# Optimization experiments

Hardware: AMD Instinct MI355X
Metric: run time of the kernel (lower is better)

The kernel has to match this reference:

```python
import jax, jax.numpy as jnp
import numpy as np

B, N, D = 8, 2048, 512

def setup_inputs() -> dict:
    key = jax.random.key(0)
    k1, k2, k3, k4, k5 = jax.random.split(key, 5)
    s = 1.0 / np.sqrt(D)
    return {
        "x": jax.random.normal(k1, (B, N, D), dtype=jnp.float32),
        "w_qkv": jax.random.normal(k2, (D, 3 * D), dtype=jnp.float32) * s,
        "b_qkv": jax.random.normal(k3, (3 * D,), dtype=jnp.float32) * 0.01,
        "w_fc": jax.random.normal(k4, (D, D), dtype=jnp.float32) * s,
        "b_fc": jax.random.normal(k5, (D,), dtype=jnp.float32) * 0.01,
    }

def reference(x, w_qkv, b_qkv, w_fc, b_fc):
    scale = 1.0 / (x.shape[-1] ** 0.5)
    qkv = x @ w_qkv + b_qkv                      # [B, N, 3D]
    q, k, v = jnp.split(qkv, 3, axis=-1)         # each [B, N, D]
    attn = jnp.einsum("bnd,bmd->bnm", q, k) * scale
    attn = jax.nn.softmax(attn, axis=-1)
    out = jnp.einsum("bnm,bmd->bnd", attn, v)
    return out @ w_fc + b_fc + x
```

## Files before the change

### kernel.cpp

```cpp
#include <hip/hip_runtime.h>
#include <stdint.h>

typedef unsigned short u16;
typedef unsigned int u32;
typedef __attribute__((ext_vector_type(8))) short short8;
typedef __attribute__((ext_vector_type(4))) float f32x4;
typedef __attribute__((ext_vector_type(8))) unsigned short u16x8;
typedef __attribute__((ext_vector_type(4))) float float4_t;

__device__ __forceinline__ float b2f(u16 u) { return __uint_as_float(((u32)u) << 16); }
__device__ __forceinline__ u16 f2b(float f) {
  u32 u = __float_as_uint(f);
  u += 0x7fffu + ((u >> 16) & 1u);
  return (u16)(u >> 16);
}

typedef const __attribute__((address_space(1))) void* gas_t;
typedef __attribute__((address_space(3))) void* las_t;
__device__ __forceinline__ void gl_lds16(const void* g, void* l) {
  __builtin_amdgcn_global_load_lds((gas_t)(uintptr_t)g, (las_t)(u32)(uintptr_t)l, 16, 0, 0);
}
__device__ __forceinline__ void barrier_pin() {
  __builtin_amdgcn_sched_barrier(0);
  __builtin_amdgcn_s_barrier();
  __builtin_amdgcn_sched_barrier(0);
}

__global__ __launch_bounds__(256) void cvt_f2b_kernel(const float* __restrict__ src,
                                                      u16* __restrict__ dst, long n) {
  long i = ((long)blockIdx.x * 256 + threadIdx.x) * 8;
  if (i >= n) return;
  float4_t v0 = *(const float4_t*)(src + i);
  float4_t v1 = *(const float4_t*)(src + i + 4);
  u16x8 o;
#pragma unroll
  for (int j = 0; j < 4; ++j) { o[j] = f2b(v0[j]); o[4 + j] = f2b(v1[j]); }
  *(u16x8*)(dst + i) = o;
}

__global__ __launch_bounds__(256) void tr_cvt(const float* __restrict__ src,
                                              u16* __restrict__ dst, int R, int C) {
  __shared__ float t[32][33];
  const int bx = blockIdx.x * 32;
  const int by = blockIdx.y * 32;
  const int tx = threadIdx.x & 31, ty = threadIdx.x >> 5;
#pragma unroll
  for (int i = 0; i < 32; i += 8)
    t[ty + i][tx] = src[(long)(by + ty + i) * C + bx + tx];
  __syncthreads();
#pragma unroll
  for (int i = 0; i < 32; i += 8)
    dst[(long)(bx + ty + i) * R + by + tx] = f2b(t[tx][ty + i]);
}

__global__ __launch_bounds__(256) void tr_v(const u16* __restrict__ qkv, u16* __restrict__ vt) {
  __shared__ u16 t[32][33];
  const int b = blockIdx.z;
  const int r0 = blockIdx.x * 32;
  const int d0 = blockIdx.y * 32;
  const int tx = threadIdx.x & 31, ty = threadIdx.x >> 5;
#pragma unroll
  for (int i = 0; i < 32; i += 8)
    t[ty + i][tx] = qkv[((long)b * 2048 + r0 + ty + i) * 1536 + 1024 + d0 + tx];
  __syncthreads();
#pragma unroll
  for (int i = 0; i < 32; i += 8)
    vt[((long)b * 512 + d0 + ty + i) * 2048 + r0 + tx] = t[tx][ty + i];
}

template <int NREP, bool OUT_F32, bool BIAS, bool RES>
__global__ __launch_bounds__(512, 1)
void gemm256(const u16* __restrict__ A, const u16* __restrict__ Bt, void* __restrict__ Cv,
             const float* __restrict__ bias, const float* __restrict__ res,
             int K, int lda, int ldb, int ldc,
             long aStride, long bStride, long cStride, float alpha) {
  __shared__ u16 As[2][256 * 64];
  __shared__ u16 Bs[2][NREP * 64 * 64];
  const int tid = threadIdx.x;
  const int wid = tid >> 6, lane = tid & 63;
  const int wr = wid >> 2, wc = wid & 3;
  const int lr = lane & 15, lg = lane >> 4;

  const int gx = gridDim.x, gy = gridDim.y;
  int id = (blockIdx.z * gy + blockIdx.y) * gx + blockIdx.x;
  const int nwg = gx * gy * gridDim.z;
  id = (id & 7) * (nwg >> 3) + (id >> 3);
  const int bxi = id % gx;
  const int t2 = id / gx;
  const int byi = t2 % gy;
  const long z = t2 / gy;

  A += z * aStride;
  Bt += z * bStride;
  const int by = byi * 256;
  const int bx = bxi * (NREP * 64);

  f32x4 acc[8][NREP] = {};
  short8 bh[NREP][2];

  const int w8l = wid * 8 + (lane >> 3);
  const int scol_src = ((lane & 7) ^ (lane >> 3)) * 8;
  const int scol_lin = (lane & 7) * 8;
  const int nT = K >> 6;
  const int sx = lane & 7;

  auto stage_A = [&](int h, int kt) {
    const int bb = kt & 1;
    const long kc = (long)kt * 64 + scol_src;
#pragma unroll
    for (int r = 0; r < 2; ++r) {
      const int row = h * 128 + r * 64 + w8l;
      gl_lds16(A + (long)(by + row) * lda + kc, &As[bb][row * 64 + scol_lin]);
    }
  };
  auto stage_Bf = [&](int kt) {
    const int bb = kt & 1;
    const long kc = (long)kt * 64 + scol_src;
#pragma unroll
    for (int r = 0; r < NREP; ++r) {
      const int row = r * 64 + w8l;
      gl_lds16(Bt + (long)(bx + row) * ldb + kc, &Bs[bb][row * 64 + scol_lin]);
    }
  };

  auto read_B = [&](int bb) {
#pragma unroll
    for (int n = 0; n < NREP; ++n) {
      const int brow = (NREP == 4) ? ((n >> 1) * 128 + wc * 32 + (n & 1) * 16 + lr)
                                   : (wc * 32 + n * 16 + lr);
#pragma unroll
      for (int ks = 0; ks < 2; ++ks)
        bh[n][ks] = *(const short8*)&Bs[bb][brow * 64 + (((ks * 4 + lg) ^ sx) * 8)];
    }
  };
  auto half_mfma = [&](int bb, int mh) {
    short8 a[4][2];
#pragma unroll
    for (int mi = 0; mi < 4; ++mi)
#pragma unroll
      for (int ks = 0; ks < 2; ++ks)
        a[mi][ks] = *(const short8*)&As[bb][(mh * 128 + wr * 64 + mi * 16 + lr) * 64 +
                                            (((ks * 4 + lg) ^ sx) * 8)];
    __builtin_amdgcn_s_setprio(1);
#pragma unroll
    for (int mi = 0; mi < 4; ++mi)
#pragma unroll
      for (int n = 0; n < NREP; ++n)
#pragma unroll
        for (int ks = 0; ks < 2; ++ks)
          acc[mh * 4 + mi][n] = __builtin_amdgcn_mfma_f32_16x16x32_bf16(
              a[mi][ks], bh[n][ks], acc[mh * 4 + mi][n], 0, 0, 0);
    __builtin_amdgcn_s_setprio(0);
  };

  stage_A(0, 0); stage_A(1, 0); stage_Bf(0);
  stage_A(0, 1);
  asm volatile("s_waitcnt vmcnt(2)" ::: "memory");
  barrier_pin();

  for (int T = 0; T < nT; T += 2) {
    const bool more = (T + 2) < nT;
    stage_A(1, T + 1); stage_Bf(T + 1);
    read_B(0); half_mfma(0, 0);
    barrier_pin();
    if (more) { stage_A(0, T + 2); stage_Bf(T + 2); }
    half_mfma(0, 1);
    if (more) {
      if constexpr (NREP == 4) asm volatile("s_waitcnt vmcnt(6)" ::: "memory");
      else                     asm volatile("s_waitcnt vmcnt(4)" ::: "memory");
    } else {
      asm volatile("s_waitcnt vmcnt(0)" ::: "memory");
    }
    barrier_pin();
    if (more) stage_A(1, T + 2);
    read_B(1); half_mfma(1, 0);
    barrier_pin();
    if (more) stage_A(0, T + 3);
    half_mfma(1, 1);
    if (more) asm volatile("s_waitcnt vmcnt(2)" ::: "memory");
    barrier_pin();
  }

  if constexpr (OUT_F32) {
    float* C = (float*)Cv + z * cStride;
#pragma unroll
    for (int mi = 0; mi < 8; ++mi)
#pragma unroll
      for (int ni = 0; ni < NREP; ++ni)
#pragma unroll
        for (int j = 0; j < 4; ++j) {
          const long row = by + (mi >> 2) * 128 + wr * 64 + (mi & 3) * 16 + lg * 4 + j;
          const int col = (NREP == 4)
                              ? bx + (ni >> 1) * 128 + wc * 32 + (ni & 1) * 16 + lr
                              : bx + wc * 32 + ni * 16 + lr;
          float v = acc[mi][ni][j] * alpha;
          if (BIAS) v += bias[col];
          if (RES) v += res[row * (long)ldc + col];
          C[row * (long)ldc + col] = v;
        }
  } else {
    u16* C = (u16*)Cv + z * cStride;
#pragma unroll
    for (int mi = 0; mi < 8; ++mi)
#pragma unroll
      for (int ni = 0; ni < NREP; ++ni)
#pragma unroll
        for (int j = 0; j < 4; ++j) {
          const long row = by + (mi >> 2) * 128 + wr * 64 + (mi & 3) * 16 + lg * 4 + j;
          const int col = (NREP == 4)
                              ? bx + (ni >> 1) * 128 + wc * 32 + (ni & 1) * 16 + lr
                              : bx + wc * 32 + ni * 16 + lr;
          float v = acc[mi][ni][j] * alpha;
          if (BIAS) v += bias[col];
          C[row * (long)ldc + col] = f2b(v);
        }
  }
}

__global__ __launch_bounds__(256) void softmax_rows(u16* __restrict__ S) {
  const long row = blockIdx.x;
  u16* p = S + row * 2048;
  const int tid = threadIdx.x;
  const int wid = tid >> 6, lane = tid & 63;
  u16x8 v = ((const u16x8*)p)[tid];
  float f[8];
#pragma unroll
  for (int j = 0; j < 8; ++j) f[j] = b2f(v[j]);
  float m = f[0];
#pragma unroll
  for (int j = 1; j < 8; ++j) m = fmaxf(m, f[j]);
#pragma unroll
  for (int off = 32; off; off >>= 1) m = fmaxf(m, __shfl_xor(m, off));
  __shared__ float rmax[4], rsum[4];
  if (lane == 0) rmax[wid] = m;
  __syncthreads();
  m = fmaxf(fmaxf(rmax[0], rmax[1]), fmaxf(rmax[2], rmax[3]));
  float s = 0.f;
#pragma unroll
  for (int j = 0; j < 8; ++j) { f[j] = __expf(f[j] - m); s += f[j]; }
#pragma unroll
  for (int off = 32; off; off >>= 1) s += __shfl_xor(s, off);
  if (lane == 0) rsum[wid] = s;
  __syncthreads();
  s = rsum[0] + rsum[1] + rsum[2] + rsum[3];
  const float inv = 1.0f / s;
  u16x8 o;
#pragma unroll
  for (int j = 0; j < 8; ++j) o[j] = f2b(f[j] * inv);
  ((u16x8*)p)[tid] = o;
}

extern "C" void kernel_launch(void* const* d_in, const int* in_sizes, int n_in,
                              void* d_out, int out_size, void* d_ws, size_t ws_size,
                              hipStream_t stream) {
  const float* x = (const float*)d_in[0];
  const float* w_qkv = (const float*)d_in[1];
  const float* b_qkv = (const float*)d_in[2];
  const float* w_fc = (const float*)d_in[3];
  const float* b_fc = (const float*)d_in[4];
  float* out = (float*)d_out;

  char* ws = (char*)d_ws;
  const long MT = 16384;
  u16* xb = (u16*)(ws);
  u16* wqkvT = (u16*)(ws + 16777216);
  u16* wfcT = (u16*)(ws + 18350080);
  u16* qkv = (u16*)(ws + 18874368);
  u16* vt = (u16*)(ws + 69206016);
  u16* S = (u16*)(ws + 85983232);
  u16* attn = xb;

  cvt_f2b_kernel<<<4096, 256, 0, stream>>>(x, xb, MT * 512);
  tr_cvt<<<dim3(48, 16), 256, 0, stream>>>(w_qkv, wqkvT, 512, 1536);
  tr_cvt<<<dim3(16, 16), 256, 0, stream>>>(w_fc, wfcT, 512, 512);

  gemm256<2, false, true, false><<<dim3(12, 64, 1), 512, 0, stream>>>(
      xb, wqkvT, qkv, b_qkv, nullptr, 512, 512, 512, 1536, 0, 0, 0, 1.0f);

  tr_v<<<dim3(64, 16, 8), 256, 0, stream>>>(qkv, vt);

  gemm256<4, false, false, false><<<dim3(8, 8, 8), 512, 0, stream>>>(
      qkv, qkv + 512, S, nullptr, nullptr, 512, 1536, 1536, 2048,
      (long)2048 * 1536, (long)2048 * 1536, (long)2048 * 2048, 0.04419417382415922f);

  softmax_rows<<<16384, 256, 0, stream>>>(S);

  gemm256<2, false, false, false><<<dim3(4, 8, 8), 512, 0, stream>>>(
      S, vt, attn, nullptr, nullptr, 2048, 2048, 2048, 512,
      (long)2048 * 2048, (long)512 * 2048, (long)2048 * 512, 1.0f);

  gemm256<2, true, true, true><<<dim3(4, 64, 1), 512, 0, stream>>>(
      attn, wfcT, out, b_fc, x, 512, 512, 512, 512, 0, 0, 0, 1.0f);
}
```

Baseline: 184.4 us.

## Separate LDS fragment reads from MFMA phases with extra barriers in GEMM loop

Splits the combined A-read-plus-MFMA step into a separate read_A phase and an mfma_half phase. Between them it adds a workgroup barrier and an explicit lgkmcnt(0) wait. The aim is a cleaner schedule in which all waves finish their LDS fragment loads before issuing a block of MFMAs, keeping LDS traffic and matrix math in distinct phases. In exchange, each K step has twice as many barriers, and the compiler can no longer overlap individual LDS reads with earlier MFMAs inside a wave.

Result: no change. 186.9 us (+1.4%).

```diff
diff --git a/kernel.cpp b/kernel.cpp
--- a/kernel.cpp
+++ b/kernel.cpp
@@ -23,6 +23,10 @@
 __device__ __forceinline__ void barrier_pin() {
   __builtin_amdgcn_sched_barrier(0);
   __builtin_amdgcn_s_barrier();
+  __builtin_amdgcn_sched_barrier(0);
+}
+__device__ __forceinline__ void lgkm0_pin() {
+  asm volatile("s_waitcnt lgkmcnt(0)" ::: "memory");
   __builtin_amdgcn_sched_barrier(0);
 }
 
@@ -97,6 +101,7 @@
 
   f32x4 acc[8][NREP] = {};
   short8 bh[NREP][2];
+  short8 ah[4][2];
 
   const int w8l = wid * 8 + (lane >> 3);
   const int scol_src = ((lane & 7) ^ (lane >> 3)) * 8;
@@ -133,14 +138,15 @@
         bh[n][ks] = *(const short8*)&Bs[bb][brow * 64 + (((ks * 4 + lg) ^ sx) * 8)];
     }
   };
-  auto half_mfma = [&](int bb, int mh) {
-    short8 a[4][2];
+  auto read_A = [&](int bb, int mh) {
 #pragma unroll
     for (int mi = 0; mi < 4; ++mi)
 #pragma unroll
       for (int ks = 0; ks < 2; ++ks)
-        a[mi][ks] = *(const short8*)&As[bb][(mh * 128 + wr * 64 + mi * 16 + lr) * 64 +
-                                            (((ks * 4 + lg) ^ sx) * 8)];
+        ah[mi][ks] = *(const short8*)&As[bb][(mh * 128 + wr * 64 + mi * 16 + lr) * 64 +
+                                             (((ks * 4 + lg) ^ sx) * 8)];
+  };
+  auto mfma_half = [&](int mh) {
     __builtin_amdgcn_s_setprio(1);
 #pragma unroll
     for (int mi = 0; mi < 4; ++mi)
@@ -149,7 +155,7 @@
 #pragma unroll
         for (int ks = 0; ks < 2; ++ks)
           acc[mh * 4 + mi][n] = __builtin_amdgcn_mfma_f32_16x16x32_bf16(
-              a[mi][ks], bh[n][ks], acc[mh * 4 + mi][n], 0, 0, 0);
+              ah[mi][ks], bh[n][ks], acc[mh * 4 + mi][n], 0, 0, 0);
     __builtin_amdgcn_s_setprio(0);
   };
 
@@ -161,10 +167,13 @@
   for (int T = 0; T < nT; T += 2) {
     const bool more = (T + 2) < nT;
     stage_A(1, T + 1); stage_Bf(T + 1);
-    read_B(0); half_mfma(0, 0);
+    read_B(0); read_A(0, 0);
+    barrier_pin();
+    lgkm0_pin();
+    mfma_half(0);
     barrier_pin();
     if (more) { stage_A(0, T + 2); stage_Bf(T + 2); }
-    half_mfma(0, 1);
+    read_A(0, 1);
     if (more) {
       if constexpr (NREP == 4) asm volatile("s_waitcnt vmcnt(6)" ::: "memory");
       else                     asm volatile("s_waitcnt vmcnt(4)" ::: "memory");
@@ -172,12 +181,21 @@
       asm volatile("s_waitcnt vmcnt(0)" ::: "memory");
     }
     barrier_pin();
+    lgkm0_pin();
+    mfma_half(1);
+    barrier_pin();
     if (more) stage_A(1, T + 2);
-    read_B(1); half_mfma(1, 0);
+    read_B(1); read_A(1, 0);
+    barrier_pin();
+    lgkm0_pin();
+    mfma_half(0);
     barrier_pin();
     if (more) stage_A(0, T + 3);
-    half_mfma(1, 1);
+    read_A(1, 1);
     if (more) asm volatile("s_waitcnt vmcnt(2)" ::: "memory");
+    barrier_pin();
+    lgkm0_pin();
+    mfma_half(1);
     barrier_pin();
   }
 
```

## Replace 256-row GEMM with 128x128 tile kernel at higher occupancy

Applied to the files above, without the earlier changes.

Swaps the 256xN-tile GEMM, which ran a split-half software pipeline, for a simpler 128x128-tile kernel with one double-buffered stage per K step. Launch bounds now allow four blocks per CU, and all four GEMM launches use grids with more blocks. The aim is better latency hiding through occupancy and more even work distribution. In exchange, each tile reuses its data less, so global/LDS traffic per FLOP is higher, and the finer-grained pipeline overlap is lost.

Result: faster. 180.0 us (-2.4%).

```diff
diff --git a/kernel.cpp b/kernel.cpp
--- a/kernel.cpp
+++ b/kernel.cpp
@@ -23,6 +23,10 @@
 __device__ __forceinline__ void barrier_pin() {
   __builtin_amdgcn_sched_barrier(0);
   __builtin_amdgcn_s_barrier();
+  __builtin_amdgcn_sched_barrier(0);
+}
+__device__ __forceinline__ void lgkm0_pin() {
+  asm volatile("s_waitcnt lgkmcnt(0)" ::: "memory");
   __builtin_amdgcn_sched_barrier(0);
 }
 
@@ -68,14 +72,14 @@
     vt[((long)b * 512 + d0 + ty + i) * 2048 + r0 + tx] = t[tx][ty + i];
 }
 
-template <int NREP, bool OUT_F32, bool BIAS, bool RES>
-__global__ __launch_bounds__(512, 1)
-void gemm256(const u16* __restrict__ A, const u16* __restrict__ Bt, void* __restrict__ Cv,
+template <bool OUT_F32, bool BIAS, bool RES>
+__global__ __launch_bounds__(512, 4)
+void gemm128(const u16* __restrict__ A, const u16* __restrict__ Bt, void* __restrict__ Cv,
              const float* __restrict__ bias, const float* __restrict__ res,
              int K, int lda, int ldb, int ldc,
              long aStride, long bStride, long cStride, float alpha) {
-  __shared__ u16 As[2][256 * 64];
-  __shared__ u16 Bs[2][NREP * 64 * 64];
+  __shared__ u16 As[2][128 * 64];
+  __shared__ u16 Bs[2][128 * 64];
   const int tid = threadIdx.x;
   const int wid = tid >> 6, lane = tid & 63;
   const int wr = wid >> 2, wc = wid & 3;
@@ -92,11 +96,11 @@
 
   A += z * aStride;
   Bt += z * bStride;
-  const int by = byi * 256;
-  const int bx = bxi * (NREP * 64);
-
-  f32x4 acc[8][NREP] = {};
-  short8 bh[NREP][2];
+  const int by = byi * 128;
+  const int bx = bxi * 128;
+
+  f32x4 acc[4][2] = {};
+  short8 ah[4][2], bh[2][2];
 
   const int w8l = wid * 8 + (lane >> 3);
   const int scol_src = ((lane & 7) ^ (lane >> 3)) * 8;
@@ -104,95 +108,66 @@
   const int nT = K >> 6;
   const int sx = lane & 7;
 
-  auto stage_A = [&](int h, int kt) {
+  auto stage = [&](int kt) {
     const int bb = kt & 1;
     const long kc = (long)kt * 64 + scol_src;
 #pragma unroll
     for (int r = 0; r < 2; ++r) {
-      const int row = h * 128 + r * 64 + w8l;
+      const int row = r * 64 + w8l;
       gl_lds16(A + (long)(by + row) * lda + kc, &As[bb][row * 64 + scol_lin]);
     }
-  };
-  auto stage_Bf = [&](int kt) {
-    const int bb = kt & 1;
-    const long kc = (long)kt * 64 + scol_src;
-#pragma unroll
-    for (int r = 0; r < NREP; ++r) {
+#pragma unroll
+    for (int r = 0; r < 2; ++r) {
       const int row = r * 64 + w8l;
       gl_lds16(Bt + (long)(bx + row) * ldb + kc, &Bs[bb][row * 64 + scol_lin]);
     }
   };
 
-  auto read_B = [&](int bb) {
-#pragma unroll
-    for (int n = 0; n < NREP; ++n) {
-      const int brow = (NREP == 4) ? ((n >> 1) * 128 + wc * 32 + (n & 1) * 16 + lr)
-                                   : (wc * 32 + n * 16 + lr);
+  stage(0);
+  asm volatile("s_waitcnt vmcnt(0)" ::: "memory");
+  barrier_pin();
+
+  for (int T = 0; T < nT; ++T) {
+    const int bb = T & 1;
+    const bool more = (T + 1) < nT;
+    if (more) stage(T + 1);
+#pragma unroll
+    for (int mi = 0; mi < 4; ++mi)
 #pragma unroll
       for (int ks = 0; ks < 2; ++ks)
-        bh[n][ks] = *(const short8*)&Bs[bb][brow * 64 + (((ks * 4 + lg) ^ sx) * 8)];
-    }
-  };
-  auto half_mfma = [&](int bb, int mh) {
-    short8 a[4][2];
-#pragma unroll
-    for (int mi = 0; mi < 4; ++mi)
+        ah[mi][ks] = *(const short8*)&As[bb][(wr * 64 + mi * 16 + lr) * 64 +
+                                             (((ks * 4 + lg) ^ sx) * 8)];
+#pragma unroll
+    for (int n = 0; n < 2; ++n)
 #pragma unroll
       for (int ks = 0; ks < 2; ++ks)
-        a[mi][ks] = *(const short8*)&As[bb][(mh * 128 + wr * 64 + mi * 16 + lr) * 64 +
+        bh[n][ks] = *(const short8*)&Bs[bb][(wc * 32 + n * 16 + lr) * 64 +
                                             (((ks * 4 + lg) ^ sx) * 8)];
+    lgkm0_pin();
     __builtin_amdgcn_s_setprio(1);
 #pragma unroll
     for (int mi = 0; mi < 4; ++mi)
 #pragma unroll
-      for (int n = 0; n < NREP; ++n)
+      for (int n = 0; n < 2; ++n)
 #pragma unroll
         for (int ks = 0; ks < 2; ++ks)
-          acc[mh * 4 + mi][n] = __builtin_amdgcn_mfma_f32_16x16x32_bf16(
-              a[mi][ks], bh[n][ks], acc[mh * 4 + mi][n], 0, 0, 0);
+          acc[mi][n] = __builtin_amdgcn_mfma_f32_16x16x32_bf16(
+              ah[mi][ks], bh[n][ks], acc[mi][n], 0, 0, 0);
     __builtin_amdgcn_s_setprio(0);
-  };
-
-  stage_A(0, 0); stage_A(1, 0); stage_Bf(0);
-  stage_A(0, 1);
-  asm volatile("s_waitcnt vmcnt(2)" ::: "memory");
-  barrier_pin();
-
-  for (int T = 0; T < nT; T += 2) {
-    const bool more = (T + 2) < nT;
-    stage_A(1, T + 1); stage_Bf(T + 1);
-    read_B(0); half_mfma(0, 0);
-    barrier_pin();
-    if (more) { stage_A(0, T + 2); stage_Bf(T + 2); }
-    half_mfma(0, 1);
-    if (more) {
-      if constexpr (NREP == 4) asm volatile("s_waitcnt vmcnt(6)" ::: "memory");
-      else                     asm volatile("s_waitcnt vmcnt(4)" ::: "memory");
-    } else {
-      asm volatile("s_waitcnt vmcnt(0)" ::: "memory");
-    }
-    barrier_pin();
-    if (more) stage_A(1, T + 2);
-    read_B(1); half_mfma(1, 0);
-    barrier_pin();
-    if (more) stage_A(0, T + 3);
-    half_mfma(1, 1);
-    if (more) asm volatile("s_waitcnt vmcnt(2)" ::: "memory");
+    if (more) asm volatile("s_waitcnt vmcnt(0)" ::: "memory");
     barrier_pin();
   }
 
   if constexpr (OUT_F32) {
     float* C = (float*)Cv + z * cStride;
 #pragma unroll
-    for (int mi = 0; mi < 8; ++mi)
-#pragma unroll
-      for (int ni = 0; ni < NREP; ++ni)
+    for (int mi = 0; mi < 4; ++mi)
+#pragma unroll
+      for (int ni = 0; ni < 2; ++ni)
 #pragma unroll
         for (int j = 0; j < 4; ++j) {
-          const long row = by + (mi >> 2) * 128 + wr * 64 + (mi & 3) * 16 + lg * 4 + j;
-          const int col = (NREP == 4)
-                              ? bx + (ni >> 1) * 128 + wc * 32 + (ni & 1) * 16 + lr
-                              : bx + wc * 32 + ni * 16 + lr;
+          const long row = by + wr * 64 + mi * 16 + lg * 4 + j;
+          const int col = bx + wc * 32 + ni * 16 + lr;
           float v = acc[mi][ni][j] * alpha;
           if (BIAS) v += bias[col];
           if (RES) v += res[row * (long)ldc + col];
@@ -201,15 +176,13 @@
   } else {
     u16* C = (u16*)Cv + z * cStride;
 #pragma unroll
-    for (int mi = 0; mi < 8; ++mi)
-#pragma unroll
-      for (int ni = 0; ni < NREP; ++ni)
+    for (int mi = 0; mi < 4; ++mi)
+#pragma unroll
+      for (int ni = 0; ni < 2; ++ni)
 #pragma unroll
         for (int j = 0; j < 4; ++j) {
-          const long row = by + (mi >> 2) * 128 + wr * 64 + (mi & 3) * 16 + lg * 4 + j;
-          const int col = (NREP == 4)
-                              ? bx + (ni >> 1) * 128 + wc * 32 + (ni & 1) * 16 + lr
-                              : bx + wc * 32 + ni * 16 + lr;
+          const long row = by + wr * 64 + mi * 16 + lg * 4 + j;
+          const int col = bx + wc * 32 + ni * 16 + lr;
           float v = acc[mi][ni][j] * alpha;
           if (BIAS) v += bias[col];
           C[row * (long)ldc + col] = f2b(v);
@@ -274,21 +247,21 @@
   tr_cvt<<<dim3(48, 16), 256, 0, stream>>>(w_qkv, wqkvT, 512, 1536);
   tr_cvt<<<dim3(16, 16), 256, 0, stream>>>(w_fc, wfcT, 512, 512);
 
-  gemm256<2, false, true, false><<<dim3(12, 64, 1), 512, 0, stream>>>(
+  gemm128<false, true, false><<<dim3(12, 128, 1), 512, 0, stream>>>(
       xb, wqkvT, qkv, b_qkv, nullptr, 512, 512, 512, 1536, 0, 0, 0, 1.0f);
 
   tr_v<<<dim3(64, 16, 8), 256, 0, stream>>>(qkv, vt);
 
-  gemm256<4, false, false, false><<<dim3(8, 8, 8), 512, 0, stream>>>(
+  gemm128<false, false, false><<<dim3(16, 16, 8), 512, 0, stream>>>(
       qkv, qkv + 512, S, nullptr, nullptr, 512, 1536, 1536, 2048,
       (long)2048 * 1536, (long)2048 * 1536, (long)2048 * 2048, 0.04419417382415922f);
 
   softmax_rows<<<16384, 256, 0, stream>>>(S);
 
-  gemm256<2, false, false, false><<<dim3(4, 8, 8), 512, 0, stream>>>(
+  gemm128<false, false, false><<<dim3(4, 16, 8), 512, 0, stream>>>(
       S, vt, attn, nullptr, nullptr, 2048, 2048, 2048, 512,
       (long)2048 * 2048, (long)512 * 2048, (long)2048 * 512, 1.0f);
 
-  gemm256<2, true, true, true><<<dim3(4, 64, 1), 512, 0, stream>>>(
+  gemm128<true, true, true><<<dim3(4, 128, 1), 512, 0, stream>>>(
       attn, wfcT, out, b_fc, x, 512, 512, 512, 512, 0, 0, 0, 1.0f);
 }
```
